# Optimization experiments

Hardware: AMD Instinct MI355X
Metric: run time of the kernel (lower is better)

## Reference

```python
import jax, jax.numpy as jnp
import numpy as np

IN_F, OUT_F = 4096, 11008
B, S = 4, 2048


def setup_inputs() -> dict:
    key = jax.random.key(0)
    k1, k2, k3, k4 = jax.random.split(key, 4)
    x = jax.random.normal(k1, (B, S, IN_F), dtype=jnp.float16)
    # int8 values in [-127, 127], carried as int32 (schema has no int8)
    int8_weights = jax.random.randint(k2, (OUT_F, IN_F), -127, 128, dtype=jnp.int32)
    # per-output-row scales: positive, small, clamped at 1e-5 like _quantize_weight
    scales = (jax.random.uniform(k3, (OUT_F, 1), dtype=jnp.float32) * 0.01 + 1e-4).astype(jnp.float16)
    bias = jax.random.normal(k4, (OUT_F,), dtype=jnp.float16)
    return {"x": x, "int8_weights": int8_weights, "scales": scales, "bias": bias}


def reference(x, int8_weights, scales, bias):
    # w8a16 GEMM: dequantize int8 weights with per-row fp16 scales, then matmul.
    x2 = x.reshape(-1, IN_F).astype(jnp.float16)            # [B*S, in]
    w = int8_weights.astype(jnp.float16) * scales            # [out, in] dequant
    out = jnp.einsum('mk,nk->mn', x2, w,
                     preferred_element_type=jnp.float16)     # [B*S, out]
    out = out + bias
    return out.reshape(B, S, OUT_F)
```

## Files before the change

### kernel.cpp

```cpp
#include <hip/hip_runtime.h>

#define M_DIM 8192
#define N_DIM 11008
#define K_DIM 4096
#define K_TILES 64

typedef __bf16 bf16x8 __attribute__((ext_vector_type(8)));
typedef float  f32x4  __attribute__((ext_vector_type(4)));
typedef int    i32x4  __attribute__((ext_vector_type(4)));
typedef unsigned short u16x8 __attribute__((ext_vector_type(8)));

__device__ __forceinline__ unsigned short f2bf_rne(float f) {
  unsigned u = __float_as_uint(f);
  u += 0x7fffu + ((u >> 16) & 1u);
  return (unsigned short)(u >> 16);
}
__device__ __forceinline__ unsigned short i2bf(int v) {
  float f = (float)v;
  return (unsigned short)(__float_as_uint(f) >> 16);
}
__device__ __forceinline__ void async_copy16(void* lds_dst, const void* g_src) {
  __builtin_amdgcn_global_load_lds(
      (const __attribute__((address_space(1))) void*)g_src,
      (__attribute__((address_space(3))) void*)lds_dst,
      16, 0, 0);
}

__global__ __launch_bounds__(256)
void dequant_w_kernel(const int* __restrict__ W, unsigned short* __restrict__ Wb) {
  const int NG = N_DIM * K_DIM / 8;
  for (int g = blockIdx.x * 256 + threadIdx.x; g < NG; g += gridDim.x * 256) {
    const int* p = W + (size_t)g * 8;
    i32x4 w0 = *(const i32x4*)p;
    i32x4 w1 = *(const i32x4*)(p + 4);
    u16x8 o;
    #pragma unroll
    for (int e = 0; e < 4; ++e) { o[e] = i2bf(w0[e]); o[e + 4] = i2bf(w1[e]); }
    *(u16x8*)(Wb + (size_t)g * 8) = o;
  }
}

__global__ __launch_bounds__(256)
void conv_x_kernel(const float* __restrict__ X, unsigned short* __restrict__ Xb) {
  const int NG = M_DIM * K_DIM / 8;
  for (int g = blockIdx.x * 256 + threadIdx.x; g < NG; g += gridDim.x * 256) {
    const float* p = X + (size_t)g * 8;
    f32x4 a0 = *(const f32x4*)p;
    f32x4 a1 = *(const f32x4*)(p + 4);
    u16x8 o;
    #pragma unroll
    for (int e = 0; e < 4; ++e) { o[e] = f2bf_rne(a0[e]); o[e + 4] = f2bf_rne(a1[e]); }
    *(u16x8*)(Xb + (size_t)g * 8) = o;
  }
}

__global__ __launch_bounds__(512, 2)
void w8a16_main_kernel(const unsigned short* __restrict__ Xb,
                       const unsigned short* __restrict__ Wb,
                       const float* __restrict__ S,
                       const float* __restrict__ Bv,
                       float*       __restrict__ O)
{
  __shared__ unsigned short sh[65536];

  const int tid  = threadIdx.x;
  const int lane = tid & 63;
  const int wid  = tid >> 6;
  const int wr   = wid >> 2;
  const int wc   = wid & 3;

  const int swz = (blockIdx.x & 7) * 172 + (blockIdx.x >> 3);
  const int bm = swz / 43, bn = swz % 43;
  const int row0 = bm * 256, col0 = bn * 256;

  f32x4 acc[8][4] = {};

  const int fr   = lane & 15;
  const int fkk  = (lane >> 4) * 8;
  const int sw_r = (fr & 7) << 3;
  const int aoff0 = fr * 64 + (fkk ^ sw_r);
  const int aoff1 = fr * 64 + ((fkk + 32) ^ sw_r);

  const int ch0 = wid * 2;
  const int sr0 = ch0 * 8 + (lane >> 3);
  const int sr1 = sr0 + 8;
  const int sc0 = ((lane & 7) * 8) ^ ((sr0 & 7) << 3);
  const int sc1 = ((lane & 7) * 8) ^ ((sr1 & 7) << 3);
  const unsigned short* Xs0 = Xb + (size_t)(row0 + sr0) * K_DIM + sc0;
  const unsigned short* Xs1 = Xb + (size_t)(row0 + sr1) * K_DIM + sc1;
  const unsigned short* Ws0 = Wb + (size_t)(col0 + sr0) * K_DIM + sc0;
  const unsigned short* Ws1 = Wb + (size_t)(col0 + sr1) * K_DIM + sc1;
  const size_t HALF = (size_t)128 * K_DIM;

#define STAGE_X(st, h) do { \
    unsigned short* _d = sh + ((st) & 1) * 32768 + (h) * 8192 + ch0 * 512; \
    async_copy16(_d,       Xs0 + (size_t)(h) * HALF + (size_t)(st) * 64); \
    async_copy16(_d + 512, Xs1 + (size_t)(h) * HALF + (size_t)(st) * 64); \
  } while (0)
#define STAGE_W(st, h) do { \
    unsigned short* _d = sh + ((st) & 1) * 32768 + 16384 + (h) * 8192 + ch0 * 512; \
    async_copy16(_d,       Ws0 + (size_t)(h) * HALF + (size_t)(st) * 64); \
    async_copy16(_d + 512, Ws1 + (size_t)(h) * HALF + (size_t)(st) * 64); \
  } while (0)

#define PHASE(tt, MQ, NQ, STAGE_STMT, VMC) do { \
    const unsigned short* Ab = sh + ((tt) & 1) * 32768; \
    const unsigned short* Bb = Ab + 16384; \
    bf16x8 af[4][2], bfv[2][2]; \
    _Pragma("unroll") \
    for (int ii = 0; ii < 4; ++ii) { \
      af[ii][0] = *(const bf16x8*)&Ab[(2 * (4 * (MQ) + ii) + wr) * 1024 + aoff0]; \
      af[ii][1] = *(const bf16x8*)&Ab[(2 * (4 * (MQ) + ii) + wr) * 1024 + aoff1]; \
    } \
    _Pragma("unroll") \
    for (int jj = 0; jj < 2; ++jj) { \
      bfv[jj][0] = *(const bf16x8*)&Bb[(4 * (2 * (NQ) + jj) + wc) * 1024 + boff0]; \
      bfv[jj][1] = *(const bf16x8*)&Bb[(4 * (2 * (NQ) + jj) + wc) * 1024 + boff1]; \
    } \
    STAGE_STMT; \
    asm volatile("s_waitcnt vmcnt(" #VMC ")" ::: "memory"); \
    __builtin_amdgcn_s_barrier(); \
    __builtin_amdgcn_s_setprio(1); \
    _Pragma("unroll") \
    for (int ii = 0; ii < 4; ++ii) \
      _Pragma("unroll") \
      for (int jj = 0; jj < 2; ++jj) { \
        acc[4*(MQ)+ii][2*(NQ)+jj] = __builtin_amdgcn_mfma_f32_16x16x32_bf16(af[ii][0], bfv[jj][0], acc[4*(MQ)+ii][2*(NQ)+jj], 0, 0, 0); \
        acc[4*(MQ)+ii][2*(NQ)+jj] = __builtin_amdgcn_mfma_f32_16x16x32_bf16(af[ii][1], bfv[jj][1], acc[4*(MQ)+ii][2*(NQ)+jj], 0, 0, 0); \
      } \
    __builtin_amdgcn_s_setprio(0); \
    __builtin_amdgcn_s_barrier(); \
    __builtin_amdgcn_sched_barrier(0); \
  } while (0)

  const int boff0 = aoff0;
  const int boff1 = aoff1;

  STAGE_X(0, 0); STAGE_W(0, 0); STAGE_W(0, 1); STAGE_X(0, 1);
  STAGE_X(1, 0); STAGE_W(1, 0);
  asm volatile("s_waitcnt vmcnt(6)" ::: "memory");
  __builtin_amdgcn_s_barrier();

  for (int i = 0; i < K_TILES / 2 - 1; ++i) {
    const int u = 2 * i, v = 2 * i + 1;
    PHASE(u, 0, 0, { STAGE_W(v, 1); },     6);
    PHASE(u, 0, 1, { STAGE_X(v, 1); },     6);
    PHASE(u, 1, 0, { STAGE_X(u + 2, 0); }, 6);
    PHASE(u, 1, 1, { STAGE_W(u + 2, 0); }, 6);
    PHASE(v, 0, 0, { STAGE_W(u + 2, 1); }, 6);
    PHASE(v, 0, 1, { STAGE_X(u + 2, 1); }, 6);
    PHASE(v, 1, 0, { STAGE_X(v + 2, 0); }, 6);
    PHASE(v, 1, 1, { STAGE_W(v + 2, 0); }, 6);
  }

  {
    const int u = K_TILES - 2, v = K_TILES - 1;
    PHASE(u, 0, 0, { STAGE_W(v, 1); }, 6);
    PHASE(u, 0, 1, { STAGE_X(v, 1); }, 4);
    PHASE(u, 1, 0, {},                 2);
    PHASE(u, 1, 1, {},                 0);
    PHASE(v, 0, 0, {},                 0);
    PHASE(v, 0, 1, {},                 0);
    PHASE(v, 1, 0, {},                 0);
    PHASE(v, 1, 1, {},                 0);
  }

  const int erow = (lane >> 4) * 4;
  const int ecol = lane & 15;
  #pragma unroll
  for (int j = 0; j < 4; ++j) {
    const int ocol = col0 + (4 * j + wc) * 16 + ecol;
    const float s  = S[ocol];
    const float bb = Bv[ocol];
    #pragma unroll
    for (int ii = 0; ii < 8; ++ii) {
      const int orow = row0 + (2 * ii + wr) * 16 + erow;
      #pragma unroll
      for (int e = 0; e < 4; ++e)
        O[(size_t)(orow + e) * N_DIM + ocol] = acc[ii][j][e] * s + bb;
    }
  }
#undef PHASE
#undef STAGE_X
#undef STAGE_W
}

#define FB_BM 128
#define FB_BK 32
#define PITCH 40
__global__ __launch_bounds__(256)
void w8a16_fallback_kernel(const float* __restrict__ X, const int* __restrict__ W,
                           const float* __restrict__ S, const float* __restrict__ Bv,
                           float* __restrict__ O)
{
  __shared__ unsigned short As[FB_BM * PITCH];
  __shared__ unsigned short Bs[FB_BM * PITCH];
  const int tid = threadIdx.x, lane = tid & 63, wid = tid >> 6;
  const int wr = wid >> 1, wc = wid & 1;
  const int p = blockIdx.x, xcd = p & 7, seq = p >> 3;
  const int bn_idx = seq >> 3, by_idx = xcd * 8 + (seq & 7);
  const int row0 = by_idx * FB_BM, col0 = bn_idx * FB_BM;
  f32x4 acc[4][4] = {};
  const int st_row = tid >> 1, st_kc = (tid & 1) * 16;
  const float* xsrc = X + (size_t)(row0 + st_row) * K_DIM + st_kc;
  const int*   wsrc = W + (size_t)(col0 + st_row) * K_DIM + st_kc;
  unsigned short* adst = &As[st_row * PITCH + st_kc];
  unsigned short* bdst = &Bs[st_row * PITCH + st_kc];
  const int fr = lane & 15, fk = (lane >> 4) * 8;
  for (int kt = 0; kt < K_DIM; kt += FB_BK) {
    f32x4 a0 = *(const f32x4*)(xsrc + kt);
    f32x4 a1 = *(const f32x4*)(xsrc + kt + 4);
    f32x4 a2 = *(const f32x4*)(xsrc + kt + 8);
    f32x4 a3 = *(const f32x4*)(xsrc + kt + 12);
    i32x4 w0 = *(const i32x4*)(wsrc + kt);
    i32x4 w1 = *(const i32x4*)(wsrc + kt + 4);
    i32x4 w2 = *(const i32x4*)(wsrc + kt + 8);
    i32x4 w3 = *(const i32x4*)(wsrc + kt + 12);
    u16x8 pa0, pa1, pb0, pb1;
    #pragma unroll
    for (int e = 0; e < 4; ++e) {
      pa0[e] = f2bf_rne(a0[e]); pa0[e+4] = f2bf_rne(a1[e]);
      pa1[e] = f2bf_rne(a2[e]); pa1[e+4] = f2bf_rne(a3[e]);
      pb0[e] = i2bf(w0[e]);     pb0[e+4] = i2bf(w1[e]);
      pb1[e] = i2bf(w2[e]);     pb1[e+4] = i2bf(w3[e]);
    }
    __syncthreads();
    *(u16x8*)(adst) = pa0; *(u16x8*)(adst + 8) = pa1;
    *(u16x8*)(bdst) = pb0; *(u16x8*)(bdst + 8) = pb1;
    __syncthreads();
    bf16x8 af[4], bfr[4];
    #pragma unroll
    for (int i = 0; i < 4; ++i)
      af[i] = *(const bf16x8*)&As[(wr * 64 + i * 16 + fr) * PITCH + fk];
    #pragma unroll
    for (int j = 0; j < 4; ++j)
      bfr[j] = *(const bf16x8*)&Bs[(wc * 64 + j * 16 + fr) * PITCH + fk];
    #pragma unroll
    for (int i = 0; i < 4; ++i)
      #pragma unroll
      for (int j = 0; j < 4; ++j)
        acc[i][j] = __builtin_amdgcn_mfma_f32_16x16x32_bf16(af[i], bfr[j], acc[i][j], 0, 0, 0);
  }
  const int erow = (lane >> 4) * 4, ecol = lane & 15;
  #pragma unroll
  for (int j = 0; j < 4; ++j) {
    const int col = col0 + wc * 64 + j * 16 + ecol;
    const float s = S[col], bb = Bv[col];
    #pragma unroll
    for (int i = 0; i < 4; ++i) {
      const int rbase = row0 + wr * 64 + i * 16 + erow;
      #pragma unroll
      for (int e = 0; e < 4; ++e)
        O[(size_t)(rbase + e) * N_DIM + col] = acc[i][j][e] * s + bb;
    }
  }
}

extern "C" void kernel_launch(void* const* d_in, const int* in_sizes, int n_in,
                              void* d_out, int out_size, void* d_ws, size_t ws_size,
                              hipStream_t stream) {
  const float* x  = (const float*)d_in[0];
  const int*   w  = (const int*)d_in[1];
  const float* sc = (const float*)d_in[2];
  const float* bi = (const float*)d_in[3];
  float* out = (float*)d_out;

  const size_t w_elems = (size_t)N_DIM * K_DIM;
  const size_t x_elems = (size_t)M_DIM * K_DIM;
  const size_t need = (w_elems + x_elems) * sizeof(unsigned short);

  if (ws_size >= need) {
    unsigned short* Wb = (unsigned short*)d_ws;
    unsigned short* Xb = Wb + w_elems;
    dequant_w_kernel<<<2048, 256, 0, stream>>>(w, Wb);
    conv_x_kernel<<<2048, 256, 0, stream>>>(x, Xb);
    const int grid = (M_DIM / 256) * (N_DIM / 256);
    w8a16_main_kernel<<<grid, 512, 0, stream>>>(Xb, Wb, sc, bi, out);
  } else {
    const int grid = (M_DIM / FB_BM) * (N_DIM / FB_BM);
    w8a16_fallback_kernel<<<grid, 256, 0, stream>>>(x, w, sc, bi, out);
  }
}
```

Before: 802.6 us.

## Reuse A/B fragments across phases with snake quadrant order and looser vmcnt

```diff
diff --git a/kernel.cpp b/kernel.cpp
--- a/kernel.cpp
+++ b/kernel.cpp
@@ -75,11 +75,16 @@
 
   f32x4 acc[8][4] = {};
 
+  bf16x8 af[4][2];
+  bf16x8 bq[2][2][2];
+
   const int fr   = lane & 15;
   const int fkk  = (lane >> 4) * 8;
   const int sw_r = (fr & 7) << 3;
   const int aoff0 = fr * 64 + (fkk ^ sw_r);
   const int aoff1 = fr * 64 + ((fkk + 32) ^ sw_r);
+  const int boff0 = aoff0;
+  const int boff1 = aoff1;
 
   const int ch0 = wid * 2;
   const int sr0 = ch0 * 8 + (lane >> 3);
@@ -103,19 +108,22 @@
     async_copy16(_d + 512, Ws1 + (size_t)(h) * HALF + (size_t)(st) * 64); \
   } while (0)
 
-#define PHASE(tt, MQ, NQ, STAGE_STMT, VMC) do { \
+#define PHASE(tt, MQ, NQ, DOA, DOB, STAGE_STMT, VMC) do { \
     const unsigned short* Ab = sh + ((tt) & 1) * 32768; \
     const unsigned short* Bb = Ab + 16384; \
-    bf16x8 af[4][2], bfv[2][2]; \
-    _Pragma("unroll") \
-    for (int ii = 0; ii < 4; ++ii) { \
-      af[ii][0] = *(const bf16x8*)&Ab[(2 * (4 * (MQ) + ii) + wr) * 1024 + aoff0]; \
-      af[ii][1] = *(const bf16x8*)&Ab[(2 * (4 * (MQ) + ii) + wr) * 1024 + aoff1]; \
+    if (DOA) { \
+      _Pragma("unroll") \
+      for (int ii = 0; ii < 4; ++ii) { \
+        af[ii][0] = *(const bf16x8*)&Ab[(2 * (4 * (MQ) + ii) + wr) * 1024 + aoff0]; \
+        af[ii][1] = *(const bf16x8*)&Ab[(2 * (4 * (MQ) + ii) + wr) * 1024 + aoff1]; \
+      } \
     } \
-    _Pragma("unroll") \
-    for (int jj = 0; jj < 2; ++jj) { \
-      bfv[jj][0] = *(const bf16x8*)&Bb[(4 * (2 * (NQ) + jj) + wc) * 1024 + boff0]; \
-      bfv[jj][1] = *(const bf16x8*)&Bb[(4 * (2 * (NQ) + jj) + wc) * 1024 + boff1]; \
+    if (DOB) { \
+      _Pragma("unroll") \
+      for (int jj = 0; jj < 2; ++jj) { \
+        bq[NQ][jj][0] = *(const bf16x8*)&Bb[(4 * (2 * (NQ) + jj) + wc) * 1024 + boff0]; \
+        bq[NQ][jj][1] = *(const bf16x8*)&Bb[(4 * (2 * (NQ) + jj) + wc) * 1024 + boff1]; \
+      } \
     } \
     STAGE_STMT; \
     asm volatile("s_waitcnt vmcnt(" #VMC ")" ::: "memory"); \
@@ -125,44 +133,41 @@
     for (int ii = 0; ii < 4; ++ii) \
       _Pragma("unroll") \
       for (int jj = 0; jj < 2; ++jj) { \
-        acc[4*(MQ)+ii][2*(NQ)+jj] = __builtin_amdgcn_mfma_f32_16x16x32_bf16(af[ii][0], bfv[jj][0], acc[4*(MQ)+ii][2*(NQ)+jj], 0, 0, 0); \
-        acc[4*(MQ)+ii][2*(NQ)+jj] = __builtin_amdgcn_mfma_f32_16x16x32_bf16(af[ii][1], bfv[jj][1], acc[4*(MQ)+ii][2*(NQ)+jj], 0, 0, 0); \
+        acc[4*(MQ)+ii][2*(NQ)+jj] = __builtin_amdgcn_mfma_f32_16x16x32_bf16(af[ii][0], bq[NQ][jj][0], acc[4*(MQ)+ii][2*(NQ)+jj], 0, 0, 0); \
+        acc[4*(MQ)+ii][2*(NQ)+jj] = __builtin_amdgcn_mfma_f32_16x16x32_bf16(af[ii][1], bq[NQ][jj][1], acc[4*(MQ)+ii][2*(NQ)+jj], 0, 0, 0); \
       } \
     __builtin_amdgcn_s_setprio(0); \
     __builtin_amdgcn_s_barrier(); \
     __builtin_amdgcn_sched_barrier(0); \
   } while (0)
 
-  const int boff0 = aoff0;
-  const int boff1 = aoff1;
-
   STAGE_X(0, 0); STAGE_W(0, 0); STAGE_W(0, 1); STAGE_X(0, 1);
   STAGE_X(1, 0); STAGE_W(1, 0);
-  asm volatile("s_waitcnt vmcnt(6)" ::: "memory");
+  asm volatile("s_waitcnt vmcnt(8)" ::: "memory");
   __builtin_amdgcn_s_barrier();
 
   for (int i = 0; i < K_TILES / 2 - 1; ++i) {
     const int u = 2 * i, v = 2 * i + 1;
-    PHASE(u, 0, 0, { STAGE_W(v, 1); },     6);
-    PHASE(u, 0, 1, { STAGE_X(v, 1); },     6);
-    PHASE(u, 1, 0, { STAGE_X(u + 2, 0); }, 6);
-    PHASE(u, 1, 1, { STAGE_W(u + 2, 0); }, 6);
-    PHASE(v, 0, 0, { STAGE_W(u + 2, 1); }, 6);
-    PHASE(v, 0, 1, { STAGE_X(u + 2, 1); }, 6);
-    PHASE(v, 1, 0, { STAGE_X(v + 2, 0); }, 6);
-    PHASE(v, 1, 1, { STAGE_W(v + 2, 0); }, 6);
+    PHASE(u, 0, 0, 1, 1, { STAGE_W(v, 1); },     8);
+    PHASE(u, 0, 1, 0, 1, { STAGE_X(v, 1); },     8);
+    PHASE(u, 1, 1, 1, 0, { STAGE_X(u + 2, 0); }, 8);
+    PHASE(u, 1, 0, 0, 0, { STAGE_W(u + 2, 0); }, 8);
+    PHASE(v, 0, 0, 1, 1, { STAGE_W(u + 2, 1); }, 8);
+    PHASE(v, 0, 1, 0, 1, { STAGE_X(u + 2, 1); }, 8);
+    PHASE(v, 1, 1, 1, 0, { STAGE_X(v + 2, 0); }, 8);
+    PHASE(v, 1, 0, 0, 0, { STAGE_W(v + 2, 0); }, 8);
   }
 
   {
     const int u = K_TILES - 2, v = K_TILES - 1;
-    PHASE(u, 0, 0, { STAGE_W(v, 1); }, 6);
-    PHASE(u, 0, 1, { STAGE_X(v, 1); }, 4);
-    PHASE(u, 1, 0, {},                 2);
-    PHASE(u, 1, 1, {},                 0);
-    PHASE(v, 0, 0, {},                 0);
-    PHASE(v, 0, 1, {},                 0);
-    PHASE(v, 1, 0, {},                 0);
-    PHASE(v, 1, 1, {},                 0);
+    PHASE(u, 0, 0, 1, 1, { STAGE_W(v, 1); }, 8);
+    PHASE(u, 0, 1, 0, 1, { STAGE_X(v, 1); }, 8);
+    PHASE(u, 1, 1, 1, 0, {},                 8);
+    PHASE(u, 1, 0, 0, 0, {},                 4);
+    PHASE(v, 0, 0, 1, 1, {},                 2);
+    PHASE(v, 0, 1, 0, 1, {},                 0);
+    PHASE(v, 1, 1, 1, 0, {},                 0);
+    PHASE(v, 1, 0, 0, 0, {},                 0);
   }
 
   const int erow = (lane >> 4) * 4;
```

Measured after the change: 717.5 us. -10.6%, faster.

## Switch main GEMM to 32x32x16 MFMA with fragment reuse across phases

Applied to the files above, without the earlier changes.

```diff
diff --git a/kernel.cpp b/kernel.cpp
--- a/kernel.cpp
+++ b/kernel.cpp
@@ -7,6 +7,7 @@
 
 typedef __bf16 bf16x8 __attribute__((ext_vector_type(8)));
 typedef float  f32x4  __attribute__((ext_vector_type(4)));
+typedef float  f32x16 __attribute__((ext_vector_type(16)));
 typedef int    i32x4  __attribute__((ext_vector_type(4)));
 typedef unsigned short u16x8 __attribute__((ext_vector_type(8)));
 
@@ -73,13 +74,18 @@
   const int bm = swz / 43, bn = swz % 43;
   const int row0 = bm * 256, col0 = bn * 256;
 
-  f32x4 acc[8][4] = {};
-
-  const int fr   = lane & 15;
-  const int fkk  = (lane >> 4) * 8;
-  const int sw_r = (fr & 7) << 3;
-  const int aoff0 = fr * 64 + (fkk ^ sw_r);
-  const int aoff1 = fr * 64 + ((fkk + 32) ^ sw_r);
+  f32x16 acc[4][2] = {};
+
+  bf16x8 af[2][4];
+  bf16x8 bq[2][4];
+
+  const int r31 = lane & 31;
+  const int kg  = (lane >> 5) * 8;
+  const int swl = (lane & 7) << 3;
+  const int off0 = r31 * 64 + ((kg)      ^ swl);
+  const int off1 = r31 * 64 + ((16 + kg) ^ swl);
+  const int off2 = r31 * 64 + ((32 + kg) ^ swl);
+  const int off3 = r31 * 64 + ((48 + kg) ^ swl);
 
   const int ch0 = wid * 2;
   const int sr0 = ch0 * 8 + (lane >> 3);
@@ -102,85 +108,89 @@
     async_copy16(_d,       Ws0 + (size_t)(h) * HALF + (size_t)(st) * 64); \
     async_copy16(_d + 512, Ws1 + (size_t)(h) * HALF + (size_t)(st) * 64); \
   } while (0)
-
-#define PHASE(tt, MQ, NQ, STAGE_STMT, VMC) do { \
+#define VM(N) asm volatile("s_waitcnt vmcnt(" #N ")" ::: "memory")
+
+#define PHASE(tt, MQ, NQ, DOA, DOB, STAGE_STMT, WAIT_STMT) do { \
     const unsigned short* Ab = sh + ((tt) & 1) * 32768; \
     const unsigned short* Bb = Ab + 16384; \
-    bf16x8 af[4][2], bfv[2][2]; \
-    _Pragma("unroll") \
-    for (int ii = 0; ii < 4; ++ii) { \
-      af[ii][0] = *(const bf16x8*)&Ab[(2 * (4 * (MQ) + ii) + wr) * 1024 + aoff0]; \
-      af[ii][1] = *(const bf16x8*)&Ab[(2 * (4 * (MQ) + ii) + wr) * 1024 + aoff1]; \
+    if (DOA) { \
+      _Pragma("unroll") \
+      for (int iq = 0; iq < 2; ++iq) { \
+        const int abase = (4 * (MQ) + 2 * iq + wr) * 2048; \
+        af[iq][0] = *(const bf16x8*)&Ab[abase + off0]; \
+        af[iq][1] = *(const bf16x8*)&Ab[abase + off1]; \
+        af[iq][2] = *(const bf16x8*)&Ab[abase + off2]; \
+        af[iq][3] = *(const bf16x8*)&Ab[abase + off3]; \
+      } \
     } \
-    _Pragma("unroll") \
-    for (int jj = 0; jj < 2; ++jj) { \
-      bfv[jj][0] = *(const bf16x8*)&Bb[(4 * (2 * (NQ) + jj) + wc) * 1024 + boff0]; \
-      bfv[jj][1] = *(const bf16x8*)&Bb[(4 * (2 * (NQ) + jj) + wc) * 1024 + boff1]; \
+    if (DOB) { \
+      const int bbase = (4 * (NQ) + wc) * 2048; \
+      bq[NQ][0] = *(const bf16x8*)&Bb[bbase + off0]; \
+      bq[NQ][1] = *(const bf16x8*)&Bb[bbase + off1]; \
+      bq[NQ][2] = *(const bf16x8*)&Bb[bbase + off2]; \
+      bq[NQ][3] = *(const bf16x8*)&Bb[bbase + off3]; \
     } \
     STAGE_STMT; \
-    asm volatile("s_waitcnt vmcnt(" #VMC ")" ::: "memory"); \
+    WAIT_STMT; \
     __builtin_amdgcn_s_barrier(); \
     __builtin_amdgcn_s_setprio(1); \
     _Pragma("unroll") \
-    for (int ii = 0; ii < 4; ++ii) \
+    for (int ks = 0; ks < 4; ++ks) \
       _Pragma("unroll") \
-      for (int jj = 0; jj < 2; ++jj) { \
-        acc[4*(MQ)+ii][2*(NQ)+jj] = __builtin_amdgcn_mfma_f32_16x16x32_bf16(af[ii][0], bfv[jj][0], acc[4*(MQ)+ii][2*(NQ)+jj], 0, 0, 0); \
-        acc[4*(MQ)+ii][2*(NQ)+jj] = __builtin_amdgcn_mfma_f32_16x16x32_bf16(af[ii][1], bfv[jj][1], acc[4*(MQ)+ii][2*(NQ)+jj], 0, 0, 0); \
-      } \
+      for (int iq = 0; iq < 2; ++iq) \
+        acc[2*(MQ)+iq][NQ] = __builtin_amdgcn_mfma_f32_32x32x16_bf16(af[iq][ks], bq[NQ][ks], acc[2*(MQ)+iq][NQ], 0, 0, 0); \
     __builtin_amdgcn_s_setprio(0); \
     __builtin_amdgcn_s_barrier(); \
     __builtin_amdgcn_sched_barrier(0); \
   } while (0)
 
-  const int boff0 = aoff0;
-  const int boff1 = aoff1;
-
   STAGE_X(0, 0); STAGE_W(0, 0); STAGE_W(0, 1); STAGE_X(0, 1);
   STAGE_X(1, 0); STAGE_W(1, 0);
-  asm volatile("s_waitcnt vmcnt(6)" ::: "memory");
+  VM(4);
   __builtin_amdgcn_s_barrier();
 
   for (int i = 0; i < K_TILES / 2 - 1; ++i) {
     const int u = 2 * i, v = 2 * i + 1;
-    PHASE(u, 0, 0, { STAGE_W(v, 1); },     6);
-    PHASE(u, 0, 1, { STAGE_X(v, 1); },     6);
-    PHASE(u, 1, 0, { STAGE_X(u + 2, 0); }, 6);
-    PHASE(u, 1, 1, { STAGE_W(u + 2, 0); }, 6);
-    PHASE(v, 0, 0, { STAGE_W(u + 2, 1); }, 6);
-    PHASE(v, 0, 1, { STAGE_X(u + 2, 1); }, 6);
-    PHASE(v, 1, 0, { STAGE_X(v + 2, 0); }, 6);
-    PHASE(v, 1, 1, { STAGE_W(v + 2, 0); }, 6);
+    PHASE(u, 0, 0, 1, 1, { STAGE_W(v, 1); },     {});
+    PHASE(u, 0, 1, 0, 1, { STAGE_X(v, 1); },     {});
+    PHASE(u, 1, 1, 1, 0, { STAGE_X(u + 2, 0); }, {});
+    PHASE(u, 1, 0, 0, 0, { STAGE_W(u + 2, 0); }, { VM(4); });
+    PHASE(v, 0, 0, 1, 1, { STAGE_W(u + 2, 1); }, {});
+    PHASE(v, 0, 1, 0, 1, { STAGE_X(u + 2, 1); }, {});
+    PHASE(v, 1, 1, 1, 0, { STAGE_X(v + 2, 0); }, {});
+    PHASE(v, 1, 0, 0, 0, { STAGE_W(v + 2, 0); }, { VM(4); });
   }
 
   {
     const int u = K_TILES - 2, v = K_TILES - 1;
-    PHASE(u, 0, 0, { STAGE_W(v, 1); }, 6);
-    PHASE(u, 0, 1, { STAGE_X(v, 1); }, 4);
-    PHASE(u, 1, 0, {},                 2);
-    PHASE(u, 1, 1, {},                 0);
-    PHASE(v, 0, 0, {},                 0);
-    PHASE(v, 0, 1, {},                 0);
-    PHASE(v, 1, 0, {},                 0);
-    PHASE(v, 1, 1, {},                 0);
-  }
-
-  const int erow = (lane >> 4) * 4;
-  const int ecol = lane & 15;
+    PHASE(u, 0, 0, 1, 1, { STAGE_W(v, 1); }, {});
+    PHASE(u, 0, 1, 0, 1, { STAGE_X(v, 1); }, {});
+    PHASE(u, 1, 1, 1, 0, {},                 {});
+    PHASE(u, 1, 0, 0, 0, {},                 { VM(4); });
+    PHASE(v, 0, 0, 1, 1, {},                 { VM(2); });
+    PHASE(v, 0, 1, 0, 1, {},                 { VM(0); });
+    PHASE(v, 1, 1, 1, 0, {},                 {});
+    PHASE(v, 1, 0, 0, 0, {},                 {});
+  }
+
+  const int rbase = (lane >> 5) * 4;
   #pragma unroll
-  for (int j = 0; j < 4; ++j) {
-    const int ocol = col0 + (4 * j + wc) * 16 + ecol;
+  for (int nq = 0; nq < 2; ++nq) {
+    const int ocol = col0 + (4 * nq + wc) * 32 + r31;
     const float s  = S[ocol];
     const float bb = Bv[ocol];
     #pragma unroll
-    for (int ii = 0; ii < 8; ++ii) {
-      const int orow = row0 + (2 * ii + wr) * 16 + erow;
+    for (int ii = 0; ii < 4; ++ii) {
+      const int orow0 = row0 + (2 * ii + wr) * 32 + rbase;
       #pragma unroll
-      for (int e = 0; e < 4; ++e)
-        O[(size_t)(orow + e) * N_DIM + ocol] = acc[ii][j][e] * s + bb;
+      for (int reg = 0; reg < 16; ++reg) {
+        const int orow = orow0 + (reg & 3) + 8 * (reg >> 2);
+        O[(size_t)orow * N_DIM + ocol] = acc[ii][nq][reg] * s + bb;
+      }
     }
   }
 #undef PHASE
+#undef VM
 #undef STAGE_X
 #undef STAGE_W
 }
@@ -228,10 +238,10 @@
     *(u16x8*)(adst) = pa0; *(u16x8*)(adst + 8) = pa1;
     *(u16x8*)(bdst) = pb0; *(u16x8*)(bdst + 8) = pb1;
     __syncthreads();
-    bf16x8 af[4], bfr[4];
+    bf16x8 af2[4], bfr[4];
     #pragma unroll
     for (int i = 0; i < 4; ++i)
-      af[i] = *(const bf16x8*)&As[(wr * 64 + i * 16 + fr) * PITCH + fk];
+      af2[i] = *(const bf16x8*)&As[(wr * 64 + i * 16 + fr) * PITCH + fk];
     #pragma unroll
     for (int j = 0; j < 4; ++j)
       bfr[j] = *(const bf16x8*)&Bs[(wc * 64 + j * 16 + fr) * PITCH + fk];
@@ -239,7 +249,7 @@
     for (int i = 0; i < 4; ++i)
       #pragma unroll
       for (int j = 0; j < 4; ++j)
-        acc[i][j] = __builtin_amdgcn_mfma_f32_16x16x32_bf16(af[i], bfr[j], acc[i][j], 0, 0, 0);
+        acc[i][j] = __builtin_amdgcn_mfma_f32_16x16x32_bf16(af2[i], bfr[j], acc[i][j], 0, 0, 0);
   }
   const int erow = (lane >> 4) * 4, ecol = lane & 15;
   #pragma unroll
```

New measurement: 799.0 us. No clear change (-0.5%).
